# Optimization experiments

Hardware: AMD Instinct MI355X
Metric: run time of the kernel (lower is better)

## Reference

```python
import jax, jax.numpy as jnp
import numpy as np
from jax import lax

# ---- static config (matches init_kwargs) ----
ORDER = 1
NPTS = ORDER + 1            # 2
JUNC_K = 300
LINE_K = 5000
NMS_SIZE = 3
JUNC_THRESH = 0.008
EPS = 1e-5
B, C, H, W = 4, 256, 160, 160
HID = C // 4                # 64
OUT_CH = [1, 1, 2, 1, 2, 4]  # lmap,jmap,joff,cmap,coff,lvec
NHEADS = len(OUT_CH)
MAXO = max(OUT_CH)          # pad conv2 out-channels to 4 per head
# channel-select indices from padded (NHEADS*MAXO) grouped-conv output
SEL = np.array([h * MAXO + c for h, k in enumerate(OUT_CH) for c in range(k)])
# lvec channel permutation from original forward (identity for order=1)
PERM = np.arange(OUT_CH[-1]).reshape(-1, 2, 2)
PERM[:, 1] = PERM[::-1, 1]
PERM = PERM.reshape(-1)


def setup_inputs() -> dict:
    key = jax.random.key(0)
    ks = jax.random.split(key, 9)
    features = jax.random.normal(ks[0], (B, C, H, W), jnp.float32)
    w1 = jax.random.normal(ks[1], (NHEADS * HID, C, 3, 3), jnp.float32) / np.sqrt(C * 9)
    b1 = 0.01 * jax.random.normal(ks[2], (NHEADS * HID,), jnp.float32)
    gamma = 1.0 + 0.1 * jax.random.normal(ks[3], (NHEADS * HID,), jnp.float32)
    beta = 0.01 * jax.random.normal(ks[4], (NHEADS * HID,), jnp.float32)
    mean = 0.1 * jax.random.normal(ks[5], (NHEADS * HID,), jnp.float32)
    var = jax.random.uniform(ks[6], (NHEADS * HID,), jnp.float32, 0.5, 1.5)
    w2 = jax.random.normal(ks[7], (NHEADS * MAXO, HID, 3, 3), jnp.float32) / np.sqrt(HID * 9)
    b2 = 0.01 * jax.random.normal(ks[8], (NHEADS * MAXO,), jnp.float32)
    return dict(features=features, w1=w1, b1=b1, gamma=gamma, beta=beta,
                mean=mean, var=var, w2=w2, b2=b2)


def _conv(x, w, b, groups=1):
    y = lax.conv_general_dilated(x, w, (1, 1), 'SAME',
                                 dimension_numbers=('NCHW', 'OIHW', 'NCHW'),
                                 feature_group_count=groups)
    return y + b[None, :, None, None]


def _nms(hm):  # hm: (1,H,W) -> suppress non-peaks
    mx = lax.reduce_window(hm, -jnp.inf, lax.max, (1, NMS_SIZE, NMS_SIZE),
                           (1, 1, 1), [(0, 0), (1, 1), (1, 1)])
    return jnp.where(hm == mx, hm, 0.0)


def _post(jm, joff, cm, coff, lv):
    """Per-sample postprocess. jm,cm:(1,H,W) joff,coff:(2,H,W) lv:(4,H,W).
    Returns (pts:(LINE_K,2,2) padded lines, mask:(LINE_K,) validity)."""
    # junctions: NMS + top-K + thresh mask + offset gather
    sj, ij = lax.top_k(_nms(jm).reshape(-1), JUNC_K)
    valid_j = sj >= JUNC_THRESH
    xy = jnp.stack([ij % W, ij // W], -1).astype(jm.dtype)
    junc = xy + joff.reshape(2, -1).T[ij] + 0.5
    junc = jnp.stack([jnp.clip(junc[:, 0], 0.0, W - 1e-4),
                      jnp.clip(junc[:, 1], 0.0, H - 1e-4)], -1)
    # lines: top-K centers + vector field gather (thresh=0 -> always full K)
    sc, ic = lax.top_k(cm.reshape(-1), LINE_K)
    cxy = jnp.stack([ic % W, ic // W], -1).astype(cm.dtype)
    center = cxy + coff.reshape(2, -1).T[ic] + 0.5
    lvr = lv.reshape(NPTS // 2 * 2, 2, -1).transpose(2, 0, 1)  # (HW,2,2)
    loi = center[:, None] + lvr[ic]                            # (L,2,2)
    loi = jnp.stack([jnp.clip(loi[..., 0], 0.0, W - 1e-4),
                     jnp.clip(loi[..., 1], 0.0, H - 1e-4)], -1)
    # pairwise squared-distance argmin of each endpoint to junctions
    d1 = ((loi[:, None, 0] - junc[None]) ** 2).sum(-1)
    d2 = ((loi[:, None, -1] - junc[None]) ** 2).sum(-1)
    big = jnp.asarray(1e18, d1.dtype)
    i1 = jnp.argmin(jnp.where(valid_j[None], d1, big), axis=-1)
    i2 = jnp.argmin(jnp.where(valid_j[None], d2, big), axis=-1)
    imin = jnp.minimum(i1, i2)
    imax = jnp.maximum(i1, i2)
    keep = imin != imax
    # unique (imin,imax) pairs via sorted-key dedup (matches torch.unique order)
    BIGK = JUNC_K * JUNC_K
    keyv = jnp.where(keep, imin * JUNC_K + imax, BIGK)
    sk = jnp.sort(keyv)
    first = jnp.concatenate([jnp.ones((1,), bool), sk[1:] != sk[:-1]]) & (sk < BIGK)
    a = jnp.where(first, sk // JUNC_K, 0)
    b = jnp.where(first, sk % JUNC_K, 0)
    pts = jnp.stack([junc[a], junc[b]], axis=1)  # (L,2,2)
    swap = pts[:, 0, 1] > pts[:, 1, 1]
    pts = jnp.where(swap[:, None, None], pts[:, ::-1], pts)
    return pts, first


def _maps(features, w1, b1, gamma, beta, mean, var, w2, b2):
    y = _conv(features, w1, b1)
    y = (y - mean[None, :, None, None]) * gamma[None, :, None, None] * \
        lax.rsqrt(var + EPS)[None, :, None, None] + beta[None, :, None, None]
    y = jax.nn.relu(y)
    y = _conv(y, w2, b2, groups=NHEADS)        # (B, NHEADS*MAXO, H, W)
    m = y[:, SEL]                              # (B, 11, H, W)
    lmap = jax.nn.sigmoid(m[:, 0:1])
    jmap = jax.nn.sigmoid(m[:, 1:2])
    joff = m[:, 2:4]
    cmap = jax.nn.sigmoid(m[:, 4:5])
    coff = m[:, 5:7]
    lvec = m[:, 7:][:, PERM]
    return lmap, jmap, joff, cmap, coff, lvec


def reference(features, w1, b1, gamma, beta, mean, var, w2, b2):
    lmap, jmap, joff, cmap, coff, lvec = _maps(features, w1, b1, gamma, beta,
                                               mean, var, w2, b2)
    loi, mask = jax.vmap(_post)(jmap, joff, cmap, coff, lvec)
    return lmap, jmap, joff, cmap, coff, lvec, loi, mask


if __name__ == '__main__':
    out = reference(**setup_inputs())
    for o in out:
        print(o.shape, o.dtype)
```

## Files before the change

### kernel.cpp

```cpp
#include <hip/hip_runtime.h>
#include <math.h>

#define IMG   160
#define HWSZ  25600
#define NB    4
#define CIN   256
#define COUT1 384
#define BIGK  90000

#define OFF_LMAP 0
#define OFF_JMAP 102400
#define OFF_JOFF 204800
#define OFF_CMAP 409600
#define OFF_COFF 512000
#define OFF_LVEC 716800
#define OFF_LOI  1126400
#define OFF_MASK 1206400

static const size_t WS_Y1    = 0;
static const size_t WS_JSORT = (size_t)NB * COUT1 * HWSZ * 4;
static const size_t WS_CSORT = WS_JSORT + (size_t)NB * 32768 * 8;
static const size_t WS_JUNC  = WS_CSORT + (size_t)NB * 32768 * 8;
static const size_t WS_JVAL  = WS_JUNC + (size_t)NB * 300 * 2 * 4;
static const size_t WS_LKEY  = WS_JVAL + (size_t)NB * 300 * 4;
static const size_t WS_WPK   = WS_LKEY + (size_t)NB * 8192 * 4;
static const size_t WS_NEED_LEGACY = WS_WPK + (size_t)12 * 8 * 9 * 32 * 64 * 2;
static const size_t WS_BNS   = WS_NEED_LEGACY;
static const size_t WS_FPK   = WS_BNS + 384 * 4;
static const size_t WS_NEED_PK = WS_FPK + (size_t)NB * 8 * 162 * 162 * 128;

typedef unsigned long long u64;
typedef __attribute__((ext_vector_type(8))) short short8;
typedef __attribute__((ext_vector_type(4))) float f32x4;
typedef __attribute__((ext_vector_type(4))) int int4v;

union frag_u { short8 s8; u64 u[2]; int4v v; };

__device__ __forceinline__ float clip_coord(float v) {
    return fminf(fmaxf(v, 0.0f), 159.9999f);
}
__device__ __forceinline__ float sigmoidf(float v) {
    return 1.0f / (1.0f + expf(-v));
}
__device__ __forceinline__ unsigned short f2bf(float f) {
    unsigned u = __float_as_uint(f);
    return (unsigned short)((u + 0x7FFFu + ((u >> 16) & 1u)) >> 16);
}
__device__ __forceinline__ float bf2f(unsigned short h) {
    return __uint_as_float((unsigned)h << 16);
}

__device__ __forceinline__ void async_copy16(void* lds, const void* g) {
    __builtin_amdgcn_global_load_lds(
        (const __attribute__((address_space(1))) unsigned int*)g,
        (__attribute__((address_space(3))) unsigned int*)lds, 16, 0, 0);
}


__global__ void bnscale_kernel(const float* __restrict__ gamma,
                               const float* __restrict__ var,
                               float* __restrict__ bns) {
    int i = blockIdx.x * 256 + threadIdx.x;
    if (i < COUT1) bns[i] = gamma[i] / sqrtf(var[i] + 1e-5f);
}

__global__ void wpack_pk_kernel(const float* __restrict__ w1, short* __restrict__ wpk) {
    int e = blockIdx.x * 256 + threadIdx.x;
    int row = e >> 6, sp = e & 63;
    int ocl = row & 31;
    int tap = (row >> 5) % 9;
    int icc = (row / 288) & 7;
    int octile = row / 2304;
    int p16 = sp >> 3, j = sp & 7;
    int l16 = p16 ^ (ocl & 7);
    int ql = l16 * 8 + j;
    int term = ql >> 5, icl = ql & 31;
    int oc = octile * 32 + ocl, ic = icc * 32 + icl;
    float a = w1[((size_t)oc * CIN + ic) * 9 + tap];
    unsigned short hi = f2bf(a);
    wpk[e] = (term == 0) ? (short)hi : (short)f2bf(a - bf2f(hi));
}

__global__ __launch_bounds__(256) void pack_feat_kernel(
    const float* __restrict__ feat, short* __restrict__ fpk) {
    const int tid = threadIdx.x;
    const int c4  = (tid >> 4) & 3;
    const int r0  = (tid & 15) | (((tid >> 6) & 3) << 4);
    const int rest = blockIdx.x * 64 + r0;
    const int px = rest % 162;
    const int t2 = rest / 162;
    const int py = t2 % 162;
    const int bi = t2 / 162;
    const int s  = (2 * py + px) & 7;
    const int gy = py - 1, gx = px - 1;
    const bool valid = ((unsigned)gy < (unsigned)IMG) && ((unsigned)gx < (unsigned)IMG);
    const float* fs = feat + (size_t)(bi * 32 + c4 * 8) * HWSZ
                           + (valid ? gy * IMG + gx : 0);
    unsigned hi4[4], lo4[4];
#pragma unroll
    for (int j2 = 0; j2 < 4; ++j2) {
        float va = valid ? fs[(size_t)(2 * j2) * HWSZ]     : 0.0f;
        float vb = valid ? fs[(size_t)(2 * j2 + 1) * HWSZ] : 0.0f;
        unsigned short ha = f2bf(va), hb = f2bf(vb);
        unsigned short la = f2bf(va - bf2f(ha)), lb = f2bf(vb - bf2f(hb));
        hi4[j2] = (unsigned)ha | ((unsigned)hb << 16);
        lo4[j2] = (unsigned)la | ((unsigned)lb << 16);
    }
    const int p0 = c4 ^ s;
    const int p1 = (c4 | 4) ^ s;
    int4v* base = (int4v*)(fpk + (size_t)rest * 64);
    base[p0] = (int4v){ (int)hi4[0], (int)hi4[1], (int)hi4[2], (int)hi4[3] };
    base[p1] = (int4v){ (int)lo4[0], (int)lo4[1], (int)lo4[2], (int)lo4[3] };
}

__global__ __launch_bounds__(256, 2) void conv1_mfma_pk(
    const short* __restrict__ fpk, const short* __restrict__ wpk,
    const float* __restrict__ b1, const float* __restrict__ bns,
    const float* __restrict__ beta, const float* __restrict__ mean,
    float* __restrict__ y1) {
    const int bid   = blockIdx.x;
    const int slot  = bid >> 3;
    const int tile  = (bid & 7) + ((slot / 12) << 3);
    const int octile = slot - (slot / 12) * 12;
    const int bb = tile / 100, tt = tile % 100;
    const int ty = (tt / 10) * 16, tx = (tt % 10) * 16;
    const int oc0 = octile * 32;
    const int tid  = threadIdx.x;
    const int w    = tid >> 6;
    const int lane = tid & 63;
    const int quad = lane >> 4;
    const int l15  = lane & 15;
    const int wbase = tid & 192;

    __shared__ __align__(16) short Alds[288 * 64];
    __shared__ __align__(16) short Blds[324 * 64];

    int aoff[2];
#pragma unroll
    for (int t = 0; t < 2; ++t)
        aoff[t] = l15 * 128 + ((((t << 2) | quad) ^ (l15 & 7)) << 4);

    f32x4 acc[2][4];
#pragma unroll
    for (int mi = 0; mi < 2; ++mi)
#pragma unroll
        for (int nj = 0; nj < 4; ++nj) acc[mi][nj] = (f32x4){0.f, 0.f, 0.f, 0.f};

    const char* asrc0 = (const char*)wpk + (size_t)(octile * 8) * 36864;

#pragma unroll 1
    for (int icc = 0; icc < 8; ++icc) {
        __syncthreads();
        {
            const char* asrc = asrc0 + (size_t)icc * 36864;
#pragma unroll
            for (int i = 0; i < 9; ++i) {
                int k = i * 256 + tid;
                async_copy16((char*)Alds + (size_t)(i * 256 + wbase) * 16,
                             asrc + (size_t)k * 16);
            }
        }
        {
            const char* bsrc = (const char*)fpk
                + (((size_t)(bb * 8 + icc) * 162 + ty) * 162 + tx) * 128;
#pragma unroll
            for (int it = 0; it < 10; ++it) {
                int k = it * 256 + tid;
                int hy = (int)((unsigned)k / 144u);
                int r  = k - hy * 144;
                async_copy16((char*)Blds + (size_t)(it * 256 + wbase) * 16,
                             bsrc + (size_t)hy * (162 * 128) + (size_t)r * 16);
            }
            if (tid < 32) {
                const int4v vv = *(const int4v*)(bsrc + (size_t)17 * (162 * 128)
                                                 + (size_t)(112 + tid) * 16);
                *(int4v*)((char*)Blds + (size_t)(2560 + tid) * 16) = vv;
            }
        }
        __syncthreads();

#pragma unroll
        for (int sx = 0; sx < 3; ++sx) {
            frag_u Bf[2][6];
#pragma unroll
            for (int t = 0; t < 2; ++t)
#pragma unroll
                for (int rr = 0; rr < 6; ++rr) {
                    int pos = (w * 4 + rr) * 18 + (l15 + sx);
                    const char* bp = (const char*)Blds + (size_t)pos * 128
                        + ((((t << 2) | quad) ^ (pos & 7)) << 4);
                    Bf[t][rr].v = *(const int4v*)bp;
                }
#pragma unroll
            for (int sy = 0; sy < 3; ++sy) {
                const int tap = sy * 3 + sx;
                frag_u Af[2][2];
#pragma unroll
                for (int t = 0; t < 2; ++t)
#pragma unroll
                    for (int mi = 0; mi < 2; ++mi) {
                        const char* ap = (const char*)Alds
                            + (size_t)(tap * 32 + mi * 16) * 128 + aoff[t];
                        Af[t][mi].v = *(const int4v*)ap;
                    }
#pragma unroll
                for (int mi = 0; mi < 2; ++mi)
#pragma unroll
                    for (int nj = 0; nj < 4; ++nj) {
                        acc[mi][nj] = __builtin_amdgcn_mfma_f32_16x16x32_bf16(
                            Af[0][mi].s8, Bf[0][nj + sy].s8, acc[mi][nj], 0, 0, 0);
                        acc[mi][nj] = __builtin_amdgcn_mfma_f32_16x16x32_bf16(
                            Af[0][mi].s8, Bf[1][nj + sy].s8, acc[mi][nj], 0, 0, 0);
                        acc[mi][nj] = __builtin_amdgcn_mfma_f32_16x16x32_bf16(
                            Af[1][mi].s8, Bf[0][nj + sy].s8, acc[mi][nj], 0, 0, 0);
                    }
            }
        }
    }

#pragma unroll
    for (int nj = 0; nj < 4; ++nj) {
        const int gy = ty + w * 4 + nj, gx = tx + l15;
#pragma unroll
        for (int mi = 0; mi < 2; ++mi)
#pragma unroll
            for (int r = 0; r < 4; ++r) {
                const int oc = oc0 + mi * 16 + quad * 4 + r;
                float v = acc[mi][nj][r] + b1[oc];
                v = (v - mean[oc]) * bns[oc] + beta[oc];
                y1[((size_t)(bb * COUT1 + oc)) * HWSZ + gy * IMG + gx] = fmaxf(v, 0.0f);
            }
    }
}


__global__ void wpack_kernel(const float* __restrict__ w1, short* __restrict__ wpk) {
    int e = blockIdx.x * 256 + threadIdx.x;
    int row = e >> 6, sp = e & 63;
    int ocl = row & 31;
    int tap = (row >> 5) % 9;
    int icc = (row / 288) & 7;
    int octile = row / 2304;
    int s = (sp >> 2) ^ (ocl & 15);
    int ql = s * 4 + (sp & 3);
    int term = ql >> 5, icl = ql & 31;
    int oc = octile * 32 + ocl, ic = icc * 32 + icl;
    float a = w1[((size_t)oc * CIN + ic) * 9 + tap];
    unsigned short hi = f2bf(a);
    wpk[e] = (term == 0) ? (short)hi : (short)f2bf(a - bf2f(hi));
}

__global__ __launch_bounds__(256, 2) void conv1_mfma(
    const float* __restrict__ feat, const short* __restrict__ wpk,
    const float* __restrict__ b1, const float* __restrict__ gamma,
    const float* __restrict__ beta, const float* __restrict__ mean,
    const float* __restrict__ var, float* __restrict__ y1) {
    const int bid   = blockIdx.x;
    const int slot  = bid >> 3;
    const int tile  = (bid & 7) + ((slot / 12) << 3);
    const int octile = slot - (slot / 12) * 12;
    const int bb = tile / 100, tt = tile % 100;
    const int ty = (tt / 10) * 16, tx = (tt % 10) * 16;
    const int oc0 = octile * 32;
    const int tid  = threadIdx.x;
    const int w    = tid >> 6;
    const int lane = tid & 63;
    const int quad = lane >> 4;
    const int l15  = lane & 15;

    __shared__ short Alds[288 * 64];
    __shared__ short Blds[324 * 68];

    int aoff[2][2];
#pragma unroll
    for (int t = 0; t < 2; ++t)
#pragma unroll
        for (int h = 0; h < 2; ++h)
            aoff[t][h] = l15 * 128 + (((t * 8 + quad * 2 + h) ^ l15) * 8);

    f32x4 acc[2][4];
#pragma unroll
    for (int mi = 0; mi < 2; ++mi)
#pragma unroll
        for (int nj = 0; nj < 4; ++nj) acc[mi][nj] = (f32x4){0.f, 0.f, 0.f, 0.f};

    const int4v* asrc_base = (const int4v*)wpk + (size_t)(octile * 8) * 2304;
    unsigned* Bd = (unsigned*)Blds;

    float pv0[21], pv1[21];

#pragma unroll
    for (int ii = 0; ii < 21; ++ii) {
        int i = tid + ii * 256;
        if (i < 5184) {
            int icp = i / 324, hp = i - icp * 324;
            int hy = hp / 18, hx = hp - hy * 18;
            int gy = ty + hy - 1, gx = tx + hx - 1;
            bool valid = ((unsigned)gy < IMG) && ((unsigned)gx < IMG);
            const float* fs = feat + ((size_t)(bb * CIN + icp * 2)) * HWSZ
                                   + (valid ? (gy * IMG + gx) : 0);
            pv0[ii] = valid ? fs[0]    : 0.0f;
            pv1[ii] = valid ? fs[HWSZ] : 0.0f;
        }
    }

#pragma unroll 1
    for (int icc = 0; icc < 8; ++icc) {
        __syncthreads();
        {
            const int4v* asrc = asrc_base + (size_t)icc * 2304;
            int4v* adst = (int4v*)Alds;
#pragma unroll
            for (int i = 0; i < 9; ++i)
                adst[tid + i * 256] = asrc[tid + i * 256];
        }
#pragma unroll
        for (int ii = 0; ii < 21; ++ii) {
            int i = tid + ii * 256;
            if (i < 5184) {
                int icp = i / 324, hp = i - icp * 324;
                float v0 = pv0[ii], v1 = pv1[ii];
                unsigned short h0 = f2bf(v0), h1 = f2bf(v1);
                unsigned short m0 = f2bf(v0 - bf2f(h0)), m1 = f2bf(v1 - bf2f(h1));
                Bd[hp * 34 + icp]      = (unsigned)h0 | ((unsigned)h1 << 16);
                Bd[hp * 34 + 16 + icp] = (unsigned)m0 | ((unsigned)m1 << 16);
            }
        }
        __syncthreads();

        if (icc < 7) {
#pragma unroll
            for (int ii = 0; ii < 21; ++ii) {
                int i = tid + ii * 256;
                if (i < 5184) {
                    int icp = i / 324, hp = i - icp * 324;
                    int hy = hp / 18, hx = hp - hy * 18;
                    int gy = ty + hy - 1, gx = tx + hx - 1;
                    bool valid = ((unsigned)gy < IMG) && ((unsigned)gx < IMG);
                    const float* fs = feat
                        + ((size_t)(bb * CIN + (icc + 1) * 32 + icp * 2)) * HWSZ
                        + (valid ? (gy * IMG + gx) : 0);
                    pv0[ii] = valid ? fs[0]    : 0.0f;
                    pv1[ii] = valid ? fs[HWSZ] : 0.0f;
                }
            }
        }

#pragma unroll
        for (int tap = 0; tap < 9; ++tap) {
            const int sy = tap / 3, sx = tap % 3;
            frag_u Af[2][2], Bf[2][4];
#pragma unroll
            for (int t = 0; t < 2; ++t) {
#pragma unroll
                for (int mi = 0; mi < 2; ++mi) {
                    const char* base = (const char*)Alds + (tap * 32 + mi * 16) * 128;
                    Af[t][mi].u[0] = *(const u64*)(base + aoff[t][0]);
                    Af[t][mi].u[1] = *(const u64*)(base + aoff[t][1]);
                }
#pragma unroll
                for (int nj = 0; nj < 4; ++nj) {
                    int pos = (w * 4 + nj + sy) * 18 + (l15 + sx);
                    const short* bp = &Blds[pos * 68 + t * 32 + quad * 8];
                    Bf[t][nj].u[0] = *(const u64*)bp;
                    Bf[t][nj].u[1] = *(const u64*)(bp + 4);
                }
            }
#pragma unroll
            for (int mi = 0; mi < 2; ++mi)
#pragma unroll
                for (int nj = 0; nj < 4; ++nj) {
                    acc[mi][nj] = __builtin_amdgcn_mfma_f32_16x16x32_bf16(
                        Af[0][mi].s8, Bf[0][nj].s8, acc[mi][nj], 0, 0, 0);
                    acc[mi][nj] = __builtin_amdgcn_mfma_f32_16x16x32_bf16(
                        Af[0][mi].s8, Bf[1][nj].s8, acc[mi][nj], 0, 0, 0);
                    acc[mi][nj] = __builtin_amdgcn_mfma_f32_16x16x32_bf16(
                        Af[1][mi].s8, Bf[0][nj].s8, acc[mi][nj], 0, 0, 0);
                    acc[mi][nj] = __builtin_amdgcn_mfma_f32_16x16x32_bf16(
                        Af[1][mi].s8, Bf[1][nj].s8, acc[mi][nj], 0, 0, 0);
                }
        }
    }

#pragma unroll
    for (int nj = 0; nj < 4; ++nj) {
        const int gy = ty + w * 4 + nj, gx = tx + l15;
#pragma unroll
        for (int mi = 0; mi < 2; ++mi)
#pragma unroll
            for (int r = 0; r < 4; ++r) {
                const int oc = oc0 + mi * 16 + quad * 4 + r;
                float v = acc[mi][nj][r] + b1[oc];
                v = (v - mean[oc]) * (gamma[oc] / sqrtf(var[oc] + 1e-5f)) + beta[oc];
                y1[((size_t)(bb * COUT1 + oc)) * HWSZ + gy * IMG + gx] = fmaxf(v, 0.0f);
            }
    }
}


__global__ __launch_bounds__(256, 2) void conv2_kernel(
    const float* __restrict__ y1, const float* __restrict__ w2,
    const float* __restrict__ b2, float* __restrict__ out) {
    const int KH[6]   = {1, 1, 2, 1, 2, 4};
    const int REG[6]  = {OFF_LMAP, OFF_JMAP, OFF_JOFF, OFF_CMAP, OFF_COFF, OFF_LVEC};
    const int SIGF[6] = {1, 1, 0, 1, 0, 0};

    const int bz = blockIdx.z;
    const int b  = bz / 6;
    const int h  = bz % 6;
    const int k  = KH[h];
    const int tx = blockIdx.x * 32, ty = blockIdx.y * 16;
    const int lx = threadIdx.x, ly = threadIdx.y;
    const int tid = ly * 16 + lx;

    __shared__ float tin[16][18][40];
    float* const tinf = &tin[0][0][0];
    float accv[4][2] = {{0.f,0.f},{0.f,0.f},{0.f,0.f},{0.f,0.f}};

    const float* yb = y1 + ((size_t)(b * COUT1 + h * 64)) * HWSZ;

    bool sok[3], sval[3];
    int  soff[3], sidx[3];
#pragma unroll
    for (int j = 0; j < 3; ++j) {
        int idx = tid + j * 256;
        sok[j] = (idx < 612);
        int r = idx / 34, col = idx - r * 34;
        int gy = ty - 1 + r, gx = tx - 1 + col;
        sval[j] = sok[j] && ((unsigned)gy < (unsigned)IMG) && ((unsigned)gx < (unsigned)IMG);
        soff[j] = sval[j] ? (gy * IMG + gx) : 0;
        sidx[j] = r * 40 + col;
    }

    for (int ic0 = 0; ic0 < 64; ic0 += 16) {
        __syncthreads();
#pragma unroll
        for (int j = 0; j < 3; ++j) {
            if (sok[j]) {
                const float* yp = yb + (size_t)ic0 * HWSZ + soff[j];
                float* tp = tinf + sidx[j];
#pragma unroll 4
                for (int c = 0; c < 16; ++c)
                    tp[c * 720] = sval[j] ? yp[(size_t)c * HWSZ] : 0.0f;
            }
        }
        __syncthreads();

        const float* tb = tinf + ly * 40 + 2 * lx;
#pragma unroll 2
        for (int c = 0; c < 16; ++c) {
            const float* tc = tb + c * 720;
            float n[3][4];
#pragma unroll
            for (int r = 0; r < 3; ++r) {
                float2 u = *(const float2*)(tc + r * 40);
                float2 v = *(const float2*)(tc + r * 40 + 2);
                n[r][0] = u.x; n[r][1] = u.y; n[r][2] = v.x; n[r][3] = v.y;
            }
#pragma unroll
            for (int o = 0; o < 4; ++o) {
                if (o < k) {
                    const float* wp = w2 + ((size_t)((h * 4 + o) * 64 + (ic0 + c))) * 9;
                    float a0 = accv[o][0], a1 = accv[o][1];
#pragma unroll
                    for (int r = 0; r < 3; ++r) {
                        float w0 = wp[3*r], w1 = wp[3*r+1], w2v = wp[3*r+2];
                        a0 = fmaf(n[r][0], w0, a0);
                        a1 = fmaf(n[r][1], w0, a1);
                        a0 = fmaf(n[r][1], w1, a0);
                        a1 = fmaf(n[r][2], w1, a1);
                        a0 = fmaf(n[r][2], w2v, a0);
                        a1 = fmaf(n[r][3], w2v, a1);
                    }
                    accv[o][0] = a0; accv[o][1] = a1;
                }
            }
        }
    }

    const int p = (ty + ly) * IMG + tx + 2 * lx;
#pragma unroll
    for (int o = 0; o < 4; ++o) {
        if (o < k) {
            float v0 = accv[o][0] + b2[h * 4 + o];
            float v1 = accv[o][1] + b2[h * 4 + o];
            if (SIGF[h]) { v0 = sigmoidf(v0); v1 = sigmoidf(v1); }
            size_t base = (size_t)REG[h] + ((size_t)(b * k + o)) * HWSZ + p;
            out[base]     = v0;
            out[base + 1] = v1;
        }
    }
}

__global__ void nms_pack_kernel(const float* __restrict__ out,
                                u64* __restrict__ jsort,
                                u64* __restrict__ csort) {
    const int g = blockIdx.x;
    const int b = g / 100, q = g % 100;
    const int p = q * 256 + threadIdx.x;
    const float* jm = out + OFF_JMAP + (size_t)b * HWSZ;
    const float* cm = out + OFF_CMAP + (size_t)b * HWSZ;

    const int x = p % IMG, y = p / IMG;
    float v = jm[p];
    float mx = v;
#pragma unroll
    for (int dy = -1; dy <= 1; ++dy)
#pragma unroll
        for (int dx = -1; dx <= 1; ++dx) {
            int nx = x + dx, ny = y + dy;
            if (nx >= 0 && nx < IMG && ny >= 0 && ny < IMG)
                mx = fmaxf(mx, jm[ny * IMG + nx]);
        }
    float nmsv = (v == mx) ? v : 0.0f;

    u64 tagj = ((u64)__float_as_uint(nmsv) << 32)
             | (u64)(0xFFFFFFFFu - (unsigned)p);
    u64 tagc = ((u64)__float_as_uint(cm[p]) << 32)
             | (u64)(0xFFFFFFFFu - (unsigned)p);
    jsort[(size_t)b * 32768 + p] = tagj;
    csort[(size_t)b * 32768 + p] = tagc;
    if (q < 28) {
        int pp = 25600 + q * 256 + threadIdx.x;
        jsort[(size_t)b * 32768 + pp] = 0ull;
        csort[(size_t)b * 32768 + pp] = 0ull;
    }
}

__global__ __launch_bounds__(1024) void sort64_ldsA(u64* __restrict__ buf) {
    __shared__ u64 s[8192];
    const size_t base = (size_t)blockIdx.x * 8192;
    const int cbase = (blockIdx.x & 3) * 8192;
    for (int i = threadIdx.x; i < 8192; i += 1024) s[i] = buf[base + i];
    for (int k = 2; k <= 8192; k <<= 1)
        for (int j = k >> 1; j > 0; j >>= 1) {
            __syncthreads();
            for (int t = threadIdx.x; t < 4096; t += 1024) {
                int i = ((t & ~(j - 1)) << 1) | (t & (j - 1));
                int l = i | j;
                bool desc = (((i + cbase) & k) == 0);
                u64 x = s[i], y = s[l];
                if (desc ? (x < y) : (x > y)) { s[i] = y; s[l] = x; }
            }
        }
    __syncthreads();
    for (int i = threadIdx.x; i < 8192; i += 1024) buf[base + i] = s[i];
}

__global__ void sort64_gstep(u64* __restrict__ buf, int k, int j) {
    int t = blockIdx.x * 256 + threadIdx.x;
    int arr = t >> 14, p = t & 16383;
    int i = ((p & ~(j - 1)) << 1) | (p & (j - 1));
    int l = i | j;
    bool desc = ((i & k) == 0);
    u64* a = buf + (size_t)arr * 32768;
    u64 x = a[i], y = a[l];
    if (desc ? (x < y) : (x > y)) { a[i] = y; a[l] = x; }
}

__global__ __launch_bounds__(1024) void sort64_ldsB(u64* __restrict__ buf, int k) {
    __shared__ u64 s[8192];
    const size_t base = (size_t)blockIdx.x * 8192;
    const int cbase = (blockIdx.x & 3) * 8192;
    for (int i = threadIdx.x; i < 8192; i += 1024) s[i] = buf[base + i];
    for (int j = 4096; j > 0; j >>= 1) {
        __syncthreads();
        for (int t = threadIdx.x; t < 4096; t += 1024) {
            int i = ((t & ~(j - 1)) << 1) | (t & (j - 1));
            int l = i | j;
            bool desc = (((i + cbase) & k) == 0);
            u64 x = s[i], y = s[l];
            if (desc ? (x < y) : (x > y)) { s[i] = y; s[l] = x; }
        }
    }
    __syncthreads();
    for (int i = threadIdx.x; i < 8192; i += 1024) buf[base + i] = s[i];
}

__global__ __launch_bounds__(1024) void sort32_lds(int* __restrict__ buf) {
    __shared__ int s[8192];
    int* a = buf + (size_t)blockIdx.x * 8192;
    for (int i = threadIdx.x; i < 8192; i += 1024) s[i] = a[i];
    for (int k = 2; k <= 8192; k <<= 1)
        for (int j = k >> 1; j > 0; j >>= 1) {
            __syncthreads();
            for (int t = threadIdx.x; t < 4096; t += 1024) {
                int i = ((t & ~(j - 1)) << 1) | (t & (j - 1));
                int l = i | j;
                bool asc = ((i & k) == 0);
                int x = s[i], y = s[l];
                if (asc ? (x > y) : (x < y)) { s[i] = y; s[l] = x; }
            }
        }
    __syncthreads();
    for (int i = threadIdx.x; i < 8192; i += 1024) a[i] = s[i];
}

__global__ void junction_kernel(const u64* __restrict__ jsort,
                                const float* __restrict__ out,
                                float* __restrict__ junc, int* __restrict__ jvalid) {
    const int b = blockIdx.x;
    const int t = threadIdx.x;
    if (t >= 300) return;
    u64 key = jsort[(size_t)b * 32768 + t];
    float score  = __uint_as_float((unsigned)(key >> 32));
    unsigned idx = 0xFFFFFFFFu - (unsigned)(key & 0xFFFFFFFFull);
    const float* j0 = out + OFF_JOFF + (size_t)(b * 2) * HWSZ;
    const float* j1 = j0 + HWSZ;
    float jx = (float)(idx % IMG) + j0[idx] + 0.5f;
    float jy = (float)(idx / IMG) + j1[idx] + 0.5f;
    junc[(size_t)(b * 300 + t) * 2]     = clip_coord(jx);
    junc[(size_t)(b * 300 + t) * 2 + 1] = clip_coord(jy);
    jvalid[b * 300 + t] = (score >= 0.008f) ? 1 : 0;
}

__global__ void lines_kernel(const u64* __restrict__ csort,
                             const float* __restrict__ junc,
                             const int* __restrict__ jvalid,
                             const float* __restrict__ out,
                             int* __restrict__ lkeys) {
    const int b = blockIdx.y;
    const int t = blockIdx.x * 256 + threadIdx.x;

    __shared__ float jx[300], jy[300];
    __shared__ int jv[300];
    for (int i = threadIdx.x; i < 300; i += 256) {
        jx[i] = junc[(size_t)(b * 300 + i) * 2];
        jy[i] = junc[(size_t)(b * 300 + i) * 2 + 1];
        jv[i] = jvalid[b * 300 + i];
    }
    __syncthreads();

    if (t >= 8192) return;
    if (t >= 5000) { lkeys[b * 8192 + t] = 0x7FFFFFFF; return; }

    u64 key = csort[(size_t)b * 32768 + t];
    unsigned idx = 0xFFFFFFFFu - (unsigned)(key & 0xFFFFFFFFull);
    const float* c0 = out + OFF_COFF + (size_t)(b * 2) * HWSZ;
    const float* c1 = c0 + HWSZ;
    const float* lv = out + OFF_LVEC + (size_t)(b * 4) * HWSZ;

    float cx = (float)(idx % IMG) + c0[idx] + 0.5f;
    float cy = (float)(idx / IMG) + c1[idx] + 0.5f;
    float e0x = clip_coord(cx + lv[idx]);
    float e0y = clip_coord(cy + lv[HWSZ + idx]);
    float e1x = clip_coord(cx + lv[2 * HWSZ + idx]);
    float e1y = clip_coord(cy + lv[3 * HWSZ + idx]);

    float m1 = 1e18f, m2 = 1e18f;
    int i1 = 0, i2 = 0;
    for (int j = 0; j < 300; ++j) {
        if (jv[j]) {
            float dx = e0x - jx[j], dy = e0y - jy[j];
            float d = dx * dx + dy * dy;
            if (d < m1) { m1 = d; i1 = j; }
            dx = e1x - jx[j]; dy = e1y - jy[j];
            d = dx * dx + dy * dy;
            if (d < m2) { m2 = d; i2 = j; }
        }
    }
    int imin = min(i1, i2), imax = max(i1, i2);
    lkeys[b * 8192 + t] = (i1 != i2) ? (imin * 300 + imax) : BIGK;
}

__global__ void finalize_kernel(const int* __restrict__ lkeys,
                                const float* __restrict__ junc,
                                float* __restrict__ out) {
    const int b = blockIdx.y;
    const int t = blockIdx.x * 256 + threadIdx.x;
    if (t >= 5000) return;
    const int* lk = lkeys + b * 8192;
    int sk = lk[t];
    bool first = ((t == 0) || (sk != lk[t - 1])) && (sk < BIGK);
    int a  = first ? sk / 300 : 0;
    int bb = first ? sk % 300 : 0;
    float p0x = junc[(size_t)(b * 300 + a) * 2];
    float p0y = junc[(size_t)(b * 300 + a) * 2 + 1];
    float p1x = junc[(size_t)(b * 300 + bb) * 2];
    float p1y = junc[(size_t)(b * 300 + bb) * 2 + 1];
    if (p0y > p1y) {
        float tx = p0x; p0x = p1x; p1x = tx;
        float ty = p0y; p0y = p1y; p1y = ty;
    }
    size_t base = OFF_LOI + (size_t)(b * 5000 + t) * 4;
    out[base]     = p0x;
    out[base + 1] = p0y;
    out[base + 2] = p1x;
    out[base + 3] = p1y;
    out[OFF_MASK + b * 5000 + t] = first ? 1.0f : 0.0f;
}

extern "C" void kernel_launch(void* const* d_in, const int* in_sizes, int n_in,
                              void* d_out, int out_size, void* d_ws, size_t ws_size,
                              hipStream_t stream) {
    const float* feat  = (const float*)d_in[0];
    const float* w1    = (const float*)d_in[1];
    const float* b1    = (const float*)d_in[2];
    const float* gamma = (const float*)d_in[3];
    const float* beta  = (const float*)d_in[4];
    const float* mean  = (const float*)d_in[5];
    const float* var   = (const float*)d_in[6];
    const float* w2    = (const float*)d_in[7];
    const float* b2    = (const float*)d_in[8];
    float* out = (float*)d_out;
    char*  ws  = (char*)d_ws;

    if (ws_size < WS_NEED_LEGACY) return;

    float* y1 = (float*)(ws + WS_Y1);
    u64* jsort = (u64*)(ws + WS_JSORT);
    float* junc = (float*)(ws + WS_JUNC);
    int* jvalid = (int*)(ws + WS_JVAL);
    int* lkeys  = (int*)(ws + WS_LKEY);
    u64* csort = (u64*)(ws + WS_CSORT);
    short* wpk = (short*)(ws + WS_WPK);
    float* bns = (float*)(ws + WS_BNS);
    short* fpk = (short*)(ws + WS_FPK);

    if (ws_size >= WS_NEED_PK) {
        wpack_pk_kernel<<<dim3(6912), dim3(256), 0, stream>>>(w1, wpk);
        bnscale_kernel<<<dim3(2), dim3(256), 0, stream>>>(gamma, var, bns);
        pack_feat_kernel<<<dim3(13122), dim3(256), 0, stream>>>(feat, fpk);
        conv1_mfma_pk<<<dim3(4800), dim3(256), 0, stream>>>(
            fpk, wpk, b1, bns, beta, mean, y1);
    } else {
        wpack_kernel<<<dim3(6912), dim3(256), 0, stream>>>(w1, wpk);
        conv1_mfma<<<dim3(4800), dim3(256), 0, stream>>>(
            feat, wpk, b1, gamma, beta, mean, var, y1);
    }

    conv2_kernel<<<dim3(5, 10, NB * 6), dim3(16, 16), 0, stream>>>(y1, w2, b2, out);

    nms_pack_kernel<<<dim3(NB * 100), dim3(256), 0, stream>>>(out, jsort, csort);

    sort64_ldsA<<<dim3(32), dim3(1024), 0, stream>>>(jsort);
    sort64_gstep<<<dim3(512), dim3(256), 0, stream>>>(jsort, 16384, 8192);
    sort64_ldsB<<<dim3(32), dim3(1024), 0, stream>>>(jsort, 16384);
    sort64_gstep<<<dim3(512), dim3(256), 0, stream>>>(jsort, 32768, 16384);
    sort64_gstep<<<dim3(512), dim3(256), 0, stream>>>(jsort, 32768, 8192);
    sort64_ldsB<<<dim3(32), dim3(1024), 0, stream>>>(jsort, 32768);

    junction_kernel<<<dim3(NB), dim3(320), 0, stream>>>(jsort, out, junc, jvalid);

    lines_kernel<<<dim3(32, NB), dim3(256), 0, stream>>>(csort, junc, jvalid, out, lkeys);

    sort32_lds<<<dim3(NB), dim3(1024), 0, stream>>>(lkeys);

    finalize_kernel<<<dim3(20, NB), dim3(256), 0, stream>>>(lkeys, junc, out);
}
```

Baseline: 967.9 us.

## Prefetch conv1 input tiles, replace global bitonic merge with rank-based top-k merge

The conv1 MFMA loop now prefetches the next input-channel chunk's feature tile into registers while the current chunk computes, and issues the next weight tile's async copy after compute, cutting one barrier per iteration. The multi-launch global bitonic sort is replaced by independent per-chunk descending sorts followed by a merge kernel. That kernel ranks each element with binary searches across the other sorted chunks and scatters only the top-K into compact buffers. The BN-scale kernel is folded into the weight-pack launch, and the LDS sort adds padding to avoid bank conflicts. This trades extra register pressure in conv1 and extra workspace for fewer kernel launches and less sorting work.

```diff
diff --git a/kernel.cpp b/kernel.cpp
--- a/kernel.cpp
+++ b/kernel.cpp
@@ -24,9 +24,12 @@
 static const size_t WS_JVAL  = WS_JUNC + (size_t)NB * 300 * 2 * 4;
 static const size_t WS_LKEY  = WS_JVAL + (size_t)NB * 300 * 4;
 static const size_t WS_WPK   = WS_LKEY + (size_t)NB * 8192 * 4;
-static const size_t WS_NEED_LEGACY = WS_WPK + (size_t)12 * 8 * 9 * 32 * 64 * 2;
-static const size_t WS_BNS   = WS_NEED_LEGACY;
-static const size_t WS_FPK   = WS_BNS + 384 * 4;
+static const size_t WS_AFTER_WPK = WS_WPK + (size_t)12 * 8 * 9 * 32 * 64 * 2;
+static const size_t WS_BNS   = WS_AFTER_WPK;
+static const size_t WS_JM    = WS_BNS + 384 * 4;
+static const size_t WS_CM    = WS_JM + (size_t)NB * 300 * 8;
+static const size_t WS_FPK   = WS_CM + (size_t)NB * 5000 * 8;
+static const size_t WS_NEED_MIN = WS_FPK;
 static const size_t WS_NEED_PK = WS_FPK + (size_t)NB * 8 * 162 * 162 * 128;
 
 typedef unsigned long long u64;
@@ -57,14 +60,15 @@
 }
 
 
-__global__ void bnscale_kernel(const float* __restrict__ gamma,
-                               const float* __restrict__ var,
-                               float* __restrict__ bns) {
-    int i = blockIdx.x * 256 + threadIdx.x;
-    if (i < COUT1) bns[i] = gamma[i] / sqrtf(var[i] + 1e-5f);
-}
-
-__global__ void wpack_pk_kernel(const float* __restrict__ w1, short* __restrict__ wpk) {
+__global__ void wpack_pk_kernel(const float* __restrict__ w1, short* __restrict__ wpk,
+                                const float* __restrict__ gamma,
+                                const float* __restrict__ var,
+                                float* __restrict__ bns) {
+    if (blockIdx.x == 6912) {
+        for (int i = threadIdx.x; i < COUT1; i += 256)
+            bns[i] = gamma[i] / sqrtf(var[i] + 1e-5f);
+        return;
+    }
     int e = blockIdx.x * 256 + threadIdx.x;
     int row = e >> 6, sp = e & 63;
     int ocl = row & 31;
@@ -148,36 +152,45 @@
 
     const char* asrc0 = (const char*)wpk + (size_t)(octile * 8) * 36864;
 
+    int boff[10];
+#pragma unroll
+    for (int it = 0; it < 10; ++it) {
+        int k = it * 256 + tid;
+        int hy = (int)((unsigned)k / 144u);
+        int r  = k - hy * 144;
+        boff[it] = hy * (162 * 128) + r * 16;
+    }
+    const int roff = 17 * (162 * 128) + (112 + (tid & 31)) * 16;
+    const char* bsrc0 = (const char*)fpk
+        + (((size_t)(bb * 8) * 162 + ty) * 162 + tx) * 128;
+    const size_t bstride = (size_t)162 * 162 * 128;
+
+    {
+#pragma unroll
+        for (int i = 0; i < 9; ++i)
+            async_copy16((char*)Alds + (size_t)(i * 256 + wbase) * 16,
+                         asrc0 + (size_t)(i * 256 + tid) * 16);
+#pragma unroll
+        for (int it = 0; it < 10; ++it)
+            async_copy16((char*)Blds + (size_t)(it * 256 + wbase) * 16,
+                         bsrc0 + boff[it]);
+        if (tid < 32) {
+            const int4v vv = *(const int4v*)(bsrc0 + roff);
+            *(int4v*)((char*)Blds + (size_t)(2560 + tid) * 16) = vv;
+        }
+    }
+    __syncthreads();
+
+    int4v pvB[10]; int4v pvR;
 #pragma unroll 1
     for (int icc = 0; icc < 8; ++icc) {
-        __syncthreads();
-        {
-            const char* asrc = asrc0 + (size_t)icc * 36864;
-#pragma unroll
-            for (int i = 0; i < 9; ++i) {
-                int k = i * 256 + tid;
-                async_copy16((char*)Alds + (size_t)(i * 256 + wbase) * 16,
-                             asrc + (size_t)k * 16);
-            }
-        }
-        {
-            const char* bsrc = (const char*)fpk
-                + (((size_t)(bb * 8 + icc) * 162 + ty) * 162 + tx) * 128;
-#pragma unroll
-            for (int it = 0; it < 10; ++it) {
-                int k = it * 256 + tid;
-                int hy = (int)((unsigned)k / 144u);
-                int r  = k - hy * 144;
-                async_copy16((char*)Blds + (size_t)(it * 256 + wbase) * 16,
-                             bsrc + (size_t)hy * (162 * 128) + (size_t)r * 16);
-            }
-            if (tid < 32) {
-                const int4v vv = *(const int4v*)(bsrc + (size_t)17 * (162 * 128)
-                                                 + (size_t)(112 + tid) * 16);
-                *(int4v*)((char*)Blds + (size_t)(2560 + tid) * 16) = vv;
-            }
-        }
-        __syncthreads();
+        if (icc < 7) {
+            const char* bs = bsrc0 + (size_t)(icc + 1) * bstride;
+#pragma unroll
+            for (int it = 0; it < 10; ++it)
+                pvB[it] = *(const int4v*)(bs + boff[it]);
+            pvR = *(const int4v*)(bs + roff);
+        }
 
 #pragma unroll
         for (int sx = 0; sx < 3; ++sx) {
@@ -215,6 +228,23 @@
                             Af[1][mi].s8, Bf[0][nj + sy].s8, acc[mi][nj], 0, 0, 0);
                     }
             }
+        }
+
+        if (icc < 7) {
+            __syncthreads();
+            {
+                const char* as = asrc0 + (size_t)(icc + 1) * 36864;
+#pragma unroll
+                for (int i = 0; i < 9; ++i)
+                    async_copy16((char*)Alds + (size_t)(i * 256 + wbase) * 16,
+                                 as + (size_t)(i * 256 + tid) * 16);
+            }
+#pragma unroll
+            for (int it = 0; it < 10; ++it)
+                *(int4v*)((char*)Blds + (size_t)(it * 256 + tid) * 16) = pvB[it];
+            if (tid < 32)
+                *(int4v*)((char*)Blds + (size_t)(2560 + tid) * 16) = pvR;
+            __syncthreads();
         }
     }
 
@@ -527,54 +557,55 @@
     }
 }
 
+#define SK64(i) ((i) + ((i) >> 4))
 __global__ __launch_bounds__(1024) void sort64_ldsA(u64* __restrict__ buf) {
-    __shared__ u64 s[8192];
+    __shared__ u64 s[8192 + 512];
     const size_t base = (size_t)blockIdx.x * 8192;
-    const int cbase = (blockIdx.x & 3) * 8192;
-    for (int i = threadIdx.x; i < 8192; i += 1024) s[i] = buf[base + i];
+    for (int i = threadIdx.x; i < 8192; i += 1024) s[SK64(i)] = buf[base + i];
     for (int k = 2; k <= 8192; k <<= 1)
         for (int j = k >> 1; j > 0; j >>= 1) {
             __syncthreads();
             for (int t = threadIdx.x; t < 4096; t += 1024) {
                 int i = ((t & ~(j - 1)) << 1) | (t & (j - 1));
                 int l = i | j;
-                bool desc = (((i + cbase) & k) == 0);
-                u64 x = s[i], y = s[l];
-                if (desc ? (x < y) : (x > y)) { s[i] = y; s[l] = x; }
+                bool desc = ((i & k) == 0);
+                u64 x = s[SK64(i)], y = s[SK64(l)];
+                if (desc ? (x < y) : (x > y)) { s[SK64(i)] = y; s[SK64(l)] = x; }
             }
         }
     __syncthreads();
-    for (int i = threadIdx.x; i < 8192; i += 1024) buf[base + i] = s[i];
-}
-
-__global__ void sort64_gstep(u64* __restrict__ buf, int k, int j) {
+    for (int i = threadIdx.x; i < 8192; i += 1024) buf[base + i] = s[SK64(i)];
+}
+
+__device__ __forceinline__ int count_gt_desc(const u64* __restrict__ a, u64 e) {
+    int cnt = 0;
+#pragma unroll
+    for (int st = 8192; st > 0; st >>= 1)
+        if (cnt + st <= 8192 && a[cnt + st - 1] > e) cnt += st;
+    return cnt;
+}
+
+__global__ void merge_topk_kernel(const u64* __restrict__ jsort,
+                                  const u64* __restrict__ csort,
+                                  u64* __restrict__ jm, u64* __restrict__ cm) {
+    const int b = blockIdx.y;
     int t = blockIdx.x * 256 + threadIdx.x;
-    int arr = t >> 14, p = t & 16383;
-    int i = ((p & ~(j - 1)) << 1) | (p & (j - 1));
-    int l = i | j;
-    bool desc = ((i & k) == 0);
-    u64* a = buf + (size_t)arr * 32768;
-    u64 x = a[i], y = a[l];
-    if (desc ? (x < y) : (x > y)) { a[i] = y; a[l] = x; }
-}
-
-__global__ __launch_bounds__(1024) void sort64_ldsB(u64* __restrict__ buf, int k) {
-    __shared__ u64 s[8192];
-    const size_t base = (size_t)blockIdx.x * 8192;
-    const int cbase = (blockIdx.x & 3) * 8192;
-    for (int i = threadIdx.x; i < 8192; i += 1024) s[i] = buf[base + i];
-    for (int j = 4096; j > 0; j >>= 1) {
-        __syncthreads();
-        for (int t = threadIdx.x; t < 4096; t += 1024) {
-            int i = ((t & ~(j - 1)) << 1) | (t & (j - 1));
-            int l = i | j;
-            bool desc = (((i + cbase) & k) == 0);
-            u64 x = s[i], y = s[l];
-            if (desc ? (x < y) : (x > y)) { s[i] = y; s[l] = x; }
-        }
-    }
-    __syncthreads();
-    for (int i = threadIdx.x; i < 8192; i += 1024) buf[base + i] = s[i];
+    const u64* src; u64* dst; int K, chunk, pos;
+    if (t < 1200) {
+        src = jsort + (size_t)b * 32768; dst = jm + (size_t)b * 300;
+        K = 300; chunk = t / 300; pos = t - chunk * 300;
+    } else {
+        t -= 1200;
+        if (t >= 20000) return;
+        src = csort + (size_t)b * 32768; dst = cm + (size_t)b * 5000;
+        K = 5000; chunk = t / 5000; pos = t - chunk * 5000;
+    }
+    u64 e = src[chunk * 8192 + pos];
+    int rank = pos;
+#pragma unroll
+    for (int c = 0; c < 4; ++c)
+        if (c != chunk) rank += count_gt_desc(src + c * 8192, e);
+    if (rank < K) dst[rank] = e;
 }
 
 __global__ __launch_bounds__(1024) void sort32_lds(int* __restrict__ buf) {
@@ -596,13 +627,13 @@
     for (int i = threadIdx.x; i < 8192; i += 1024) a[i] = s[i];
 }
 
-__global__ void junction_kernel(const u64* __restrict__ jsort,
+__global__ void junction_kernel(const u64* __restrict__ jmk,
                                 const float* __restrict__ out,
                                 float* __restrict__ junc, int* __restrict__ jvalid) {
     const int b = blockIdx.x;
     const int t = threadIdx.x;
     if (t >= 300) return;
-    u64 key = jsort[(size_t)b * 32768 + t];
+    u64 key = jmk[(size_t)b * 300 + t];
     float score  = __uint_as_float((unsigned)(key >> 32));
     unsigned idx = 0xFFFFFFFFu - (unsigned)(key & 0xFFFFFFFFull);
     const float* j0 = out + OFF_JOFF + (size_t)(b * 2) * HWSZ;
@@ -614,7 +645,7 @@
     jvalid[b * 300 + t] = (score >= 0.008f) ? 1 : 0;
 }
 
-__global__ void lines_kernel(const u64* __restrict__ csort,
+__global__ void lines_kernel(const u64* __restrict__ cmk,
                              const float* __restrict__ junc,
                              const int* __restrict__ jvalid,
                              const float* __restrict__ out,
@@ -634,7 +665,7 @@
     if (t >= 8192) return;
     if (t >= 5000) { lkeys[b * 8192 + t] = 0x7FFFFFFF; return; }
 
-    u64 key = csort[(size_t)b * 32768 + t];
+    u64 key = cmk[(size_t)b * 5000 + t];
     unsigned idx = 0xFFFFFFFFu - (unsigned)(key & 0xFFFFFFFFull);
     const float* c0 = out + OFF_COFF + (size_t)(b * 2) * HWSZ;
     const float* c1 = c0 + HWSZ;
@@ -705,7 +736,7 @@
     float* out = (float*)d_out;
     char*  ws  = (char*)d_ws;
 
-    if (ws_size < WS_NEED_LEGACY) return;
+    if (ws_size < WS_NEED_MIN) return;
 
     float* y1 = (float*)(ws + WS_Y1);
     u64* jsort = (u64*)(ws + WS_JSORT);
@@ -715,11 +746,12 @@
     u64* csort = (u64*)(ws + WS_CSORT);
     short* wpk = (short*)(ws + WS_WPK);
     float* bns = (float*)(ws + WS_BNS);
+    u64* jm    = (u64*)(ws + WS_JM);
+    u64* cm    = (u64*)(ws + WS_CM);
     short* fpk = (short*)(ws + WS_FPK);
 
     if (ws_size >= WS_NEED_PK) {
-        wpack_pk_kernel<<<dim3(6912), dim3(256), 0, stream>>>(w1, wpk);
-        bnscale_kernel<<<dim3(2), dim3(256), 0, stream>>>(gamma, var, bns);
+        wpack_pk_kernel<<<dim3(6913), dim3(256), 0, stream>>>(w1, wpk, gamma, var, bns);
         pack_feat_kernel<<<dim3(13122), dim3(256), 0, stream>>>(feat, fpk);
         conv1_mfma_pk<<<dim3(4800), dim3(256), 0, stream>>>(
             fpk, wpk, b1, bns, beta, mean, y1);
@@ -734,15 +766,12 @@
     nms_pack_kernel<<<dim3(NB * 100), dim3(256), 0, stream>>>(out, jsort, csort);
 
     sort64_ldsA<<<dim3(32), dim3(1024), 0, stream>>>(jsort);
-    sort64_gstep<<<dim3(512), dim3(256), 0, stream>>>(jsort, 16384, 8192);
-    sort64_ldsB<<<dim3(32), dim3(1024), 0, stream>>>(jsort, 16384);
-    sort64_gstep<<<dim3(512), dim3(256), 0, stream>>>(jsort, 32768, 16384);
-    sort64_gstep<<<dim3(512), dim3(256), 0, stream>>>(jsort, 32768, 8192);
-    sort64_ldsB<<<dim3(32), dim3(1024), 0, stream>>>(jsort, 32768);
-
-    junction_kernel<<<dim3(NB), dim3(320), 0, stream>>>(jsort, out, junc, jvalid);
-
-    lines_kernel<<<dim3(32, NB), dim3(256), 0, stream>>>(csort, junc, jvalid, out, lkeys);
+
+    merge_topk_kernel<<<dim3(83, NB), dim3(256), 0, stream>>>(jsort, csort, jm, cm);
+
+    junction_kernel<<<dim3(NB), dim3(320), 0, stream>>>(jm, out, junc, jvalid);
+
+    lines_kernel<<<dim3(32, NB), dim3(256), 0, stream>>>(cm, junc, jvalid, out, lkeys);
 
     sort32_lds<<<dim3(NB), dim3(1024), 0, stream>>>(lkeys);
 
```

New measurement: 950.4 us. No clear change (-1.8%).
